# Optimization experiments

Measured on AMD Instinct MI355X. Metric: run time of the kernel, lower is better.

Reference implementation:

```python
import jax, jax.numpy as jnp
import numpy as np

B, C, H, W = 16, 128, 112, 112
OUTC = 256


def _conv(x, w, padding, groups=1, bias=None):
    y = jax.lax.conv_general_dilated(
        x, w, window_strides=(1, 1), padding=[(padding, padding), (padding, padding)],
        dimension_numbers=("NCHW", "OIHW", "NCHW"), feature_group_count=groups)
    if bias is not None:
        y = y + bias[None, :, None, None]
    return y


def _grid_sample_1ch(chan, g):
    # chan: [B,H,W] single channel; g: [B,H,W,2] with (x,y) in [-1,1].
    # PyTorch grid_sample: bilinear, zeros padding, align_corners=False.
    Bn, Hc, Wc = chan.shape
    ix = (g[..., 0] + 1.0) * (Wc * 0.5) - 0.5
    iy = (g[..., 1] + 1.0) * (Hc * 0.5) - 0.5
    x0 = jnp.floor(ix)
    y0 = jnp.floor(iy)
    wx = ix - x0
    wy = iy - y0
    x0i = x0.astype(jnp.int32)
    y0i = y0.astype(jnp.int32)
    flat = chan.reshape(Bn, -1)

    def gather(yi, xi):
        valid = (yi >= 0) & (yi < Hc) & (xi >= 0) & (xi < Wc)
        idx = jnp.clip(yi, 0, Hc - 1) * Wc + jnp.clip(xi, 0, Wc - 1)
        v = jnp.take_along_axis(flat, idx.reshape(Bn, -1), axis=1).reshape(idx.shape)
        return jnp.where(valid, v, 0.0)

    v00 = gather(y0i, x0i)
    v01 = gather(y0i, x0i + 1)
    v10 = gather(y0i + 1, x0i)
    v11 = gather(y0i + 1, x0i + 1)
    return (v00 * (1 - wx) * (1 - wy) + v01 * wx * (1 - wy)
            + v10 * (1 - wx) * wy + v11 * wx * wy)


def setup_inputs() -> dict:
    key = jax.random.key(0)
    k1, k2, k3, k4 = jax.random.split(key, 4)
    x = jax.random.normal(k1, (B, C, H, W), dtype=jnp.float32)
    depth_w = jax.random.normal(k2, (C, 1, 3, 3), dtype=jnp.float32) * 0.1
    point_w = jax.random.normal(k3, (OUTC, C, 1, 1), dtype=jnp.float32) * 0.05
    offset_w = jax.random.normal(k4, (2 * C, C, 3, 3), dtype=jnp.float32) * 0.02
    offset_b = jnp.zeros((2 * C,), dtype=jnp.float32)
    return {"x": x, "depth_w": depth_w, "point_w": point_w,
            "offset_w": offset_w, "offset_b": offset_b}


def reference(x, depth_w, point_w, offset_w, offset_b):
    offset = jnp.tanh(_conv(x, offset_w, padding=1, bias=offset_b))  # [B,2C,H,W]
    out = _conv(x, depth_w, padding=1, groups=C)                     # [B,C,H,W]

    # Base grid, matching np.meshgrid + np.repeat([C,C], axis=0):
    # channels 0..C-1 are all X, channels C..2C-1 are all Y.
    gX, gY = jnp.meshgrid(jnp.linspace(-1.0, 1.0, W), jnp.linspace(-1.0, 1.0, H), indexing="xy")
    grid = jnp.concatenate([gX[None], gY[None]], axis=0)  # [2,H,W]
    grid = jnp.repeat(grid, C, axis=0)                    # [2C,H,W]

    sg = jnp.clip(grid[None] + offset, -1.0, 1.0)         # [B,2C,H,W]
    sg = sg.transpose(0, 2, 3, 1)                         # [B,H,W,2C]
    sg = sg.reshape(B, H, W, C, 2).transpose(3, 0, 1, 2, 4)  # [C,B,H,W,2]

    chans = out.transpose(1, 0, 2, 3)                     # [C,B,H,W]
    sampled = jax.vmap(_grid_sample_1ch)(chans, sg)       # [C,B,H,W]
    sampled = sampled.transpose(1, 0, 2, 3)               # [B,C,H,W]

    return _conv(sampled, point_w, padding=0)             # [B,OUTC,H,W]
```

## Files before the change

### kernel.cpp

```cpp
#include <hip/hip_runtime.h>
#include <hip/hip_bf16.h>

#define B_    16
#define C_    128
#define H_    112
#define W_    112
#define OUTC_ 256
#define TWOC_ 256
#define HW_   (H_ * W_)
#define CHW_  ((size_t)C_ * HW_)

typedef __hip_bfloat16 bf16;
typedef short bf16x8 __attribute__((ext_vector_type(8)));
typedef short s16x4  __attribute__((ext_vector_type(4)));
typedef float f32x4  __attribute__((ext_vector_type(4)));

__device__ __forceinline__ float b2f(bf16 v) { return __bfloat162float(v); }
__device__ __forceinline__ bf16  f2b(float v) { return __float2bfloat16(v); }

__device__ __forceinline__ float rd(const float* p) { return *p; }
__device__ __forceinline__ float rd(const bf16* p)  { return b2f(*p); }
__device__ __forceinline__ void  wr(float* p, float v) { *p = v; }
__device__ __forceinline__ void  wr(bf16* p,  float v) { *p = f2b(v); }

__device__ __forceinline__ float fast_tanh(float v) {
    float e = __expf(2.f * v);
    return 1.f - 2.f / (e + 1.f);
}

__global__ __launch_bounds__(256) void k_probe(const unsigned short* __restrict__ x,
                                               int* __restrict__ flag) {
    __shared__ int cnt[256];
    int tid = threadIdx.x;
    int c = 0;
#pragma unroll
    for (int i = 0; i < 8; ++i) {
        unsigned short u = x[tid * 8 + i];
        int e = (u >> 7) & 0xFF;
        if (e >= 135) c++;
    }
    cnt[tid] = c;
    __syncthreads();
    if (tid == 0) {
        int s = 0;
        for (int i = 0; i < 256; ++i) s += cnt[i];
        *flag = (s > 64) ? 1 : 0;
    }
}

__global__ __launch_bounds__(256) void k_wprep(const void* __restrict__ ow,
                                               bf16* __restrict__ wth,
                                               bf16* __restrict__ wtl,
                                               const int* __restrict__ flag) {
    int i = blockIdx.x * 256 + threadIdx.x;
    if (i >= 9 * 4 * 256 * 32) return;
    int cp  = i & 31;
    int oc  = (i >> 5) & 255;
    int tcc = i >> 13;
    int cc  = tcc & 3;
    int tap = tcc >> 2;
    int c   = cc * 32 + cp;
    size_t src = ((size_t)oc * C_ + c) * 9 + tap;
    float v = (*flag) ? ((const float*)ow)[src] : b2f(((const bf16*)ow)[src]);
    bf16 hb = f2b(v);
    float lo = v - b2f(hb);
    wth[i] = hb;
    wtl[i] = f2b(lo);
}

__global__ __launch_bounds__(256) void k_pwprep(const void* __restrict__ pw,
                                                bf16* __restrict__ pwh,
                                                bf16* __restrict__ pwl,
                                                const int* __restrict__ flag) {
    int i = blockIdx.x * 256 + threadIdx.x;
    if (i >= 4 * 256 * 32) return;
    int cp   = i & 31;
    int oc   = (i >> 5) & 255;
    int cc   = i >> 13;
    int c    = cc * 32 + cp;
    size_t src = (size_t)oc * C_ + c;
    float v = (*flag) ? ((const float*)pw)[src] : b2f(((const bf16*)pw)[src]);
    bf16 hb = f2b(v);
    float lo = v - b2f(hb);
    pwh[i] = hb;
    pwl[i] = f2b(lo);
}

__global__ __launch_bounds__(256) void k_offset_mfma(
    const void* __restrict__ xsrc, const bf16* __restrict__ wth,
    const bf16* __restrict__ wtl, const void* __restrict__ ob,
    float* __restrict__ off, const int* __restrict__ flag)
{
    __shared__ alignas(16) short Sh[114 * 32];
    __shared__ alignas(16) short Sl[114 * 32];

    const int tid  = threadIdx.x;
    const int lane = tid & 63;
    const int wv   = tid >> 6;
    const int l15  = lane & 15;
    const int l4   = lane >> 4;
    const int hraw = blockIdx.x;
    const int h    = (hraw & 7) * 14 + (hraw >> 3);
    const int b    = blockIdx.y;
    const int fullp = *flag;

    const float* xf = (const float*)xsrc;
    const bf16*  xb = (const bf16*)xsrc;

    f32x4 acc[4][7];
    f32x4 zero = {0.f, 0.f, 0.f, 0.f};
#pragma unroll
    for (int m = 0; m < 4; ++m)
#pragma unroll
        for (int n = 0; n < 7; ++n) acc[m][n] = zero;

    for (int cc = 0; cc < 4; ++cc) {
        for (int kh = 0; kh < 3; ++kh) {
            const int row = h + kh - 1;
            const bool rowok = (row >= 0) && (row < H_);
            __syncthreads();
            for (int i = tid; i < 912; i += 256) {
                int n  = i % 114;
                int cq = i / 114;
                int col = n - 1;
                bool ok = rowok && (col >= 0) && (col < W_);
                size_t base = ((size_t)(b * C_ + cc * 32 + cq * 4)) * HW_
                            + (size_t)row * W_ + col;
                short hs[4], ls[4];
#pragma unroll
                for (int t = 0; t < 4; ++t) {
                    float v = 0.f;
                    if (ok) v = fullp ? xf[base + (size_t)t * HW_]
                                      : b2f(xb[base + (size_t)t * HW_]);
                    bf16 hb = f2b(v);
                    float hv = b2f(hb);
                    bf16 lb = f2b(v - hv);
                    hs[t] = *(short*)&hb;
                    ls[t] = *(short*)&lb;
                }
                int ob_ = (cq * 8) ^ (((n >> 1) & 3) << 4);
                int so  = n * 32 + (ob_ >> 1);
                s16x4 th, tl;
                th[0] = hs[0]; th[1] = hs[1]; th[2] = hs[2]; th[3] = hs[3];
                tl[0] = ls[0]; tl[1] = ls[1]; tl[2] = ls[2]; tl[3] = ls[3];
                *(s16x4*)&Sh[so] = th;
                *(s16x4*)&Sl[so] = tl;
            }
            __syncthreads();

            for (int kw = 0; kw < 3; ++kw) {
                const size_t wchunk = ((size_t)((kh * 3 + kw) * 4 + cc)) * (256 * 32);
                bf16x8 ah[4], al[4];
#pragma unroll
                for (int m = 0; m < 4; ++m) {
                    size_t aoff = (size_t)(wv * 64 + m * 16 + l15) * 32 + 8 * l4;
                    ah[m] = *(const bf16x8*)(wth + wchunk + aoff);
                }
                if (fullp) {
#pragma unroll
                    for (int m = 0; m < 4; ++m) {
                        size_t aoff = (size_t)(wv * 64 + m * 16 + l15) * 32 + 8 * l4;
                        al[m] = *(const bf16x8*)(wtl + wchunk + aoff);
                    }
                }
#pragma unroll
                for (int n = 0; n < 7; ++n) {
                    int rowb = n * 16 + l15 + kw;
                    int o2   = (16 * l4) ^ (((rowb >> 1) & 3) << 4);
                    int so   = rowb * 32 + (o2 >> 1);
                    bf16x8 xh = *(const bf16x8*)&Sh[so];
#pragma unroll
                    for (int m = 0; m < 4; ++m)
                        acc[m][n] = __builtin_amdgcn_mfma_f32_16x16x32_bf16(
                            ah[m], xh, acc[m][n], 0, 0, 0);
                    if (fullp) {
                        bf16x8 xl = *(const bf16x8*)&Sl[so];
#pragma unroll
                        for (int m = 0; m < 4; ++m)
                            acc[m][n] = __builtin_amdgcn_mfma_f32_16x16x32_bf16(
                                ah[m], xl, acc[m][n], 0, 0, 0);
#pragma unroll
                        for (int m = 0; m < 4; ++m)
                            acc[m][n] = __builtin_amdgcn_mfma_f32_16x16x32_bf16(
                                al[m], xh, acc[m][n], 0, 0, 0);
                    }
                }
            }
        }
    }

#pragma unroll
    for (int m = 0; m < 4; ++m) {
        int ocb = wv * 64 + m * 16 + l4 * 4;
        float bias[4];
#pragma unroll
        for (int j = 0; j < 4; ++j)
            bias[j] = fullp ? ((const float*)ob)[ocb + j]
                            : b2f(((const bf16*)ob)[ocb + j]);
#pragma unroll
        for (int n = 0; n < 7; ++n) {
            int w = n * 16 + l15;
#pragma unroll
            for (int j = 0; j < 4; ++j) {
                size_t o = ((size_t)(b * TWOC_ + ocb + j)) * HW_ + (size_t)h * W_ + w;
                off[o] = fast_tanh(acc[m][n][j] + bias[j]);
            }
        }
    }
}

template <typename TI>
__device__ void dw_body(const TI* __restrict__ x, const TI* __restrict__ dw,
                        bf16* __restrict__ out) {
    int hw = blockIdx.x * 256 + threadIdx.x;
    int c = blockIdx.y, b = blockIdx.z;
    int h = hw / W_, w = hw - h * W_;
    float wv[9];
#pragma unroll
    for (int k = 0; k < 9; ++k) wv[k] = rd(dw + c * 9 + k);
    const TI* xc = x + (size_t)b * CHW_ + (size_t)c * HW_;
    float acc = 0.f;
#pragma unroll
    for (int kh = 0; kh < 3; ++kh) {
        int hh = h + kh - 1;
        bool hv = (hh >= 0) && (hh < H_);
#pragma unroll
        for (int kw = 0; kw < 3; ++kw) {
            int ww = w + kw - 1;
            bool v = hv && (ww >= 0) && (ww < W_);
            acc += (v ? rd(xc + hh * W_ + ww) : 0.f) * wv[kh * 3 + kw];
        }
    }
    out[(size_t)(b * C_ + c) * HW_ + hw] = f2b(acc);
}

__global__ __launch_bounds__(256) void k_dw(const void* x, const void* dw,
                                            bf16* out, const int* flag) {
    if (*flag) dw_body<float>((const float*)x, (const float*)dw, out);
    else       dw_body<bf16>((const bf16*)x, (const bf16*)dw, out);
}

__global__ __launch_bounds__(256) void k_sample(
    const float* __restrict__ off, const bf16* __restrict__ dwout,
    bf16* __restrict__ samp) {
    int hw = blockIdx.x * 256 + threadIdx.x;
    int c = blockIdx.y, b = blockIdx.z;
    int h = hw / W_, w = hw - h * W_;

    float gbase = (c < 64) ? (-1.f + 2.f * (float)w / 111.f)
                           : (-1.f + 2.f * (float)h / 111.f);
    const float* offb = off + (size_t)b * TWOC_ * HW_;
    float ox = offb[(size_t)(2 * c) * HW_ + hw];
    float oy = offb[(size_t)(2 * c + 1) * HW_ + hw];
    float gx = fminf(fmaxf(gbase + ox, -1.f), 1.f);
    float gy = fminf(fmaxf(gbase + oy, -1.f), 1.f);
    float ix = (gx + 1.f) * 56.f - 0.5f;
    float iy = (gy + 1.f) * 56.f - 0.5f;
    float x0f = floorf(ix), y0f = floorf(iy);
    float wx = ix - x0f, wy = iy - y0f;
    int x0 = (int)x0f, y0 = (int)y0f;

    const bf16* p = dwout + (size_t)(b * C_ + c) * HW_;
    float v00 = 0.f, v01 = 0.f, v10 = 0.f, v11 = 0.f;
    bool y0v = (y0 >= 0) && (y0 < H_), y1v = (y0 + 1 >= 0) && (y0 + 1 < H_);
    bool x0v = (x0 >= 0) && (x0 < W_), x1v = (x0 + 1 >= 0) && (x0 + 1 < W_);
    if (y0v && x0v) v00 = b2f(p[y0 * W_ + x0]);
    if (y0v && x1v) v01 = b2f(p[y0 * W_ + x0 + 1]);
    if (y1v && x0v) v10 = b2f(p[(y0 + 1) * W_ + x0]);
    if (y1v && x1v) v11 = b2f(p[(y0 + 1) * W_ + x0 + 1]);

    float v = v00 * (1.f - wx) * (1.f - wy) + v01 * wx * (1.f - wy)
            + v10 * (1.f - wx) * wy + v11 * wx * wy;
    samp[(size_t)(b * C_ + c) * HW_ + hw] = f2b(v);
}

__global__ __launch_bounds__(256) void k_pw_mfma(
    const bf16* __restrict__ samp, const bf16* __restrict__ pwh,
    const bf16* __restrict__ pwl, void* __restrict__ out,
    const int* __restrict__ flag)
{
    const int tid  = threadIdx.x;
    const int lane = tid & 63;
    const int wv   = tid >> 6;
    const int l15  = lane & 15;
    const int l4   = lane >> 4;
    const int hraw = blockIdx.x;
    const int h    = (hraw & 7) * 14 + (hraw >> 3);
    const int b    = blockIdx.y;
    const int fullp = *flag;

    const bf16* srow = samp + (size_t)b * C_ * HW_ + (size_t)h * W_;

    f32x4 acc[4][7];
    f32x4 zero = {0.f, 0.f, 0.f, 0.f};
#pragma unroll
    for (int m = 0; m < 4; ++m)
#pragma unroll
        for (int n = 0; n < 7; ++n) acc[m][n] = zero;

    for (int cc = 0; cc < 4; ++cc) {
        bf16x8 ah[4], al[4];
#pragma unroll
        for (int m = 0; m < 4; ++m) {
            size_t aoff = ((size_t)cc * 256 + (wv * 64 + m * 16 + l15)) * 32 + 8 * l4;
            ah[m] = *(const bf16x8*)(pwh + aoff);
        }
        if (fullp) {
#pragma unroll
            for (int m = 0; m < 4; ++m) {
                size_t aoff = ((size_t)cc * 256 + (wv * 64 + m * 16 + l15)) * 32 + 8 * l4;
                al[m] = *(const bf16x8*)(pwl + aoff);
            }
        }
#pragma unroll
        for (int n = 0; n < 7; ++n) {
            int w = n * 16 + l15;
            const bf16* bp = srow + (size_t)(cc * 32 + 8 * l4) * HW_ + w;
            bf16x8 xv;
#pragma unroll
            for (int j = 0; j < 8; ++j) {
                bf16 t = bp[(size_t)j * HW_];
                xv[j] = *(short*)&t;
            }
#pragma unroll
            for (int m = 0; m < 4; ++m)
                acc[m][n] = __builtin_amdgcn_mfma_f32_16x16x32_bf16(
                    ah[m], xv, acc[m][n], 0, 0, 0);
            if (fullp) {
#pragma unroll
                for (int m = 0; m < 4; ++m)
                    acc[m][n] = __builtin_amdgcn_mfma_f32_16x16x32_bf16(
                        al[m], xv, acc[m][n], 0, 0, 0);
            }
        }
    }

#pragma unroll
    for (int m = 0; m < 4; ++m) {
        int ocb = wv * 64 + m * 16 + l4 * 4;
#pragma unroll
        for (int n = 0; n < 7; ++n) {
            int w = n * 16 + l15;
#pragma unroll
            for (int j = 0; j < 4; ++j) {
                size_t o = ((size_t)(b * OUTC_ + ocb + j)) * HW_ + (size_t)h * W_ + w;
                if (fullp) ((float*)out)[o] = acc[m][n][j];
                else       ((bf16*)out)[o]  = f2b(acc[m][n][j]);
            }
        }
    }
}

extern "C" void kernel_launch(void* const* d_in, const int* in_sizes, int n_in,
                              void* d_out, int out_size, void* d_ws, size_t ws_size,
                              hipStream_t stream) {
    (void)in_sizes; (void)n_in; (void)out_size; (void)ws_size;
    const void* x        = d_in[0];
    const void* depth_w  = d_in[1];
    const void* point_w  = d_in[2];
    const void* offset_w = d_in[3];
    const void* offset_b = d_in[4];

    char* ws = (char*)d_ws;
    int*   flag = (int*)ws;
    const size_t off_bytes = (size_t)B_ * TWOC_ * HW_ * 4;
    float* off  = (float*)(ws + 256);
    bf16*  wth  = (bf16*)(ws + 256 + off_bytes);
    bf16*  wtl  = wth + 9 * 4 * 256 * 32;
    bf16*  pwh  = wtl + 9 * 4 * 256 * 32;
    bf16*  pwl  = pwh + 4 * 256 * 32;
    bf16* dwout = pwl + 4 * 256 * 32;
    bf16* samp  = dwout + (size_t)B_ * C_ * HW_;

    k_probe      <<<1, 256, 0, stream>>>((const unsigned short*)x, flag);
    k_wprep      <<<1152, 256, 0, stream>>>(offset_w, wth, wtl, flag);
    k_pwprep     <<<128, 256, 0, stream>>>(point_w, pwh, pwl, flag);
    k_offset_mfma<<<dim3(H_, B_), 256, 0, stream>>>(x, wth, wtl, offset_b, off, flag);
    k_dw         <<<dim3(49, C_, B_), 256, 0, stream>>>(x, depth_w, dwout, flag);
    k_sample     <<<dim3(49, C_, B_), 256, 0, stream>>>(off, dwout, samp);
    k_pw_mfma    <<<dim3(H_, B_), 256, 0, stream>>>(samp, pwh, pwl, d_out, flag);
}
```

Baseline: 1.041 ms.

## Double-buffer offset conv input staging and stage pointwise input via LDS

```diff
diff --git a/kernel.cpp b/kernel.cpp
--- a/kernel.cpp
+++ b/kernel.cpp
@@ -20,8 +20,6 @@
 
 __device__ __forceinline__ float rd(const float* p) { return *p; }
 __device__ __forceinline__ float rd(const bf16* p)  { return b2f(*p); }
-__device__ __forceinline__ void  wr(float* p, float v) { *p = v; }
-__device__ __forceinline__ void  wr(bf16* p,  float v) { *p = f2b(v); }
 
 __device__ __forceinline__ float fast_tanh(float v) {
     float e = __expf(2.f * v);
@@ -91,8 +89,8 @@
     const bf16* __restrict__ wtl, const void* __restrict__ ob,
     float* __restrict__ off, const int* __restrict__ flag)
 {
-    __shared__ alignas(16) short Sh[114 * 32];
-    __shared__ alignas(16) short Sl[114 * 32];
+    __shared__ alignas(16) short Sh[2][114 * 32];
+    __shared__ alignas(16) short Sl[2][114 * 32];
 
     const int tid  = threadIdx.x;
     const int lane = tid & 63;
@@ -107,6 +105,17 @@
     const float* xf = (const float*)xsrc;
     const bf16*  xb = (const bf16*)xsrc;
 
+    int  nn[4], cq[4];
+    bool act[4];
+#pragma unroll
+    for (int t = 0; t < 4; ++t) {
+        int i = tid + 256 * t;
+        act[t] = (i < 912);
+        int ii = act[t] ? i : 0;
+        nn[t] = ii % 114;
+        cq[t] = ii / 114;
+    }
+
     f32x4 acc[4][7];
     f32x4 zero = {0.f, 0.f, 0.f, 0.f};
 #pragma unroll
@@ -114,79 +123,104 @@
 #pragma unroll
         for (int n = 0; n < 7; ++n) acc[m][n] = zero;
 
-    for (int cc = 0; cc < 4; ++cc) {
-        for (int kh = 0; kh < 3; ++kh) {
-            const int row = h + kh - 1;
-            const bool rowok = (row >= 0) && (row < H_);
-            __syncthreads();
-            for (int i = tid; i < 912; i += 256) {
-                int n  = i % 114;
-                int cq = i / 114;
-                int col = n - 1;
-                bool ok = rowok && (col >= 0) && (col < W_);
-                size_t base = ((size_t)(b * C_ + cc * 32 + cq * 4)) * HW_
-                            + (size_t)row * W_ + col;
-                short hs[4], ls[4];
-#pragma unroll
-                for (int t = 0; t < 4; ++t) {
-                    float v = 0.f;
-                    if (ok) v = fullp ? xf[base + (size_t)t * HW_]
-                                      : b2f(xb[base + (size_t)t * HW_]);
-                    bf16 hb = f2b(v);
-                    float hv = b2f(hb);
-                    bf16 lb = f2b(v - hv);
-                    hs[t] = *(short*)&hb;
-                    ls[t] = *(short*)&lb;
-                }
-                int ob_ = (cq * 8) ^ (((n >> 1) & 3) << 4);
-                int so  = n * 32 + (ob_ >> 1);
-                s16x4 th, tl;
-                th[0] = hs[0]; th[1] = hs[1]; th[2] = hs[2]; th[3] = hs[3];
-                tl[0] = ls[0]; tl[1] = ls[1]; tl[2] = ls[2]; tl[3] = ls[3];
-                *(s16x4*)&Sh[so] = th;
-                *(s16x4*)&Sl[so] = tl;
-            }
-            __syncthreads();
-
-            for (int kw = 0; kw < 3; ++kw) {
-                const size_t wchunk = ((size_t)((kh * 3 + kw) * 4 + cc)) * (256 * 32);
-                bf16x8 ah[4], al[4];
+    float vreg[4][4];
+
+    auto issue = [&](int s) {
+        int cc = s >> 2;
+        int kh = s - cc * 3;
+        cc = s / 3; kh = s - cc * 3;
+        int row = h + kh - 1;
+        bool rowok = (row >= 0) && (row < H_);
+#pragma unroll
+        for (int t = 0; t < 4; ++t) {
+            int col = nn[t] - 1;
+            bool ok = act[t] && rowok && (col >= 0) && (col < W_);
+            size_t base = ((size_t)(b * C_ + cc * 32 + cq[t] * 4)) * HW_
+                        + (size_t)row * W_ + col;
+#pragma unroll
+            for (int q = 0; q < 4; ++q) {
+                float v = 0.f;
+                if (ok) v = fullp ? xf[base + (size_t)q * HW_]
+                                  : b2f(xb[base + (size_t)q * HW_]);
+                vreg[t][q] = v;
+            }
+        }
+    };
+
+    auto writebuf = [&](int bi) {
+#pragma unroll
+        for (int t = 0; t < 4; ++t) {
+            if (!act[t]) continue;
+            short hs[4], ls[4];
+#pragma unroll
+            for (int q = 0; q < 4; ++q) {
+                float v = vreg[t][q];
+                bf16 hb = f2b(v);
+                float hv = b2f(hb);
+                bf16 lb = f2b(v - hv);
+                hs[q] = *(short*)&hb;
+                ls[q] = *(short*)&lb;
+            }
+            int n   = nn[t];
+            int ob_ = (cq[t] * 8) ^ (((n >> 1) & 3) << 4);
+            int so  = n * 32 + (ob_ >> 1);
+            s16x4 th, tl;
+            th[0] = hs[0]; th[1] = hs[1]; th[2] = hs[2]; th[3] = hs[3];
+            tl[0] = ls[0]; tl[1] = ls[1]; tl[2] = ls[2]; tl[3] = ls[3];
+            *(s16x4*)&Sh[bi][so] = th;
+            *(s16x4*)&Sl[bi][so] = tl;
+        }
+    };
+
+    issue(0);
+    writebuf(0);
+
+    for (int s = 0; s < 12; ++s) {
+        const int cc = s / 3;
+        const int kh = s - cc * 3;
+        if (s < 11) issue(s + 1);
+        __syncthreads();
+        const short* Bh = Sh[s & 1];
+        const short* Bl = Sl[s & 1];
+        for (int kw = 0; kw < 3; ++kw) {
+            const size_t wchunk = ((size_t)((kh * 3 + kw) * 4 + cc)) * (256 * 32);
+            bf16x8 ah[4], al[4];
+#pragma unroll
+            for (int m = 0; m < 4; ++m) {
+                size_t aoff = (size_t)(wv * 64 + m * 16 + l15) * 32 + 8 * l4;
+                ah[m] = *(const bf16x8*)(wth + wchunk + aoff);
+            }
+            if (fullp) {
 #pragma unroll
                 for (int m = 0; m < 4; ++m) {
                     size_t aoff = (size_t)(wv * 64 + m * 16 + l15) * 32 + 8 * l4;
-                    ah[m] = *(const bf16x8*)(wth + wchunk + aoff);
+                    al[m] = *(const bf16x8*)(wtl + wchunk + aoff);
                 }
+            }
+#pragma unroll
+            for (int n = 0; n < 7; ++n) {
+                int rowb = n * 16 + l15 + kw;
+                int o2   = (16 * l4) ^ (((rowb >> 1) & 3) << 4);
+                int so   = rowb * 32 + (o2 >> 1);
+                bf16x8 xh = *(const bf16x8*)&Bh[so];
+#pragma unroll
+                for (int m = 0; m < 4; ++m)
+                    acc[m][n] = __builtin_amdgcn_mfma_f32_16x16x32_bf16(
+                        ah[m], xh, acc[m][n], 0, 0, 0);
                 if (fullp) {
-#pragma unroll
-                    for (int m = 0; m < 4; ++m) {
-                        size_t aoff = (size_t)(wv * 64 + m * 16 + l15) * 32 + 8 * l4;
-                        al[m] = *(const bf16x8*)(wtl + wchunk + aoff);
-                    }
-                }
-#pragma unroll
-                for (int n = 0; n < 7; ++n) {
-                    int rowb = n * 16 + l15 + kw;
-                    int o2   = (16 * l4) ^ (((rowb >> 1) & 3) << 4);
-                    int so   = rowb * 32 + (o2 >> 1);
-                    bf16x8 xh = *(const bf16x8*)&Sh[so];
+                    bf16x8 xl = *(const bf16x8*)&Bl[so];
 #pragma unroll
                     for (int m = 0; m < 4; ++m)
                         acc[m][n] = __builtin_amdgcn_mfma_f32_16x16x32_bf16(
-                            ah[m], xh, acc[m][n], 0, 0, 0);
-                    if (fullp) {
-                        bf16x8 xl = *(const bf16x8*)&Sl[so];
-#pragma unroll
-                        for (int m = 0; m < 4; ++m)
-                            acc[m][n] = __builtin_amdgcn_mfma_f32_16x16x32_bf16(
-                                ah[m], xl, acc[m][n], 0, 0, 0);
-#pragma unroll
-                        for (int m = 0; m < 4; ++m)
-                            acc[m][n] = __builtin_amdgcn_mfma_f32_16x16x32_bf16(
-                                al[m], xh, acc[m][n], 0, 0, 0);
-                    }
+                            ah[m], xl, acc[m][n], 0, 0, 0);
+#pragma unroll
+                    for (int m = 0; m < 4; ++m)
+                        acc[m][n] = __builtin_amdgcn_mfma_f32_16x16x32_bf16(
+                            al[m], xh, acc[m][n], 0, 0, 0);
                 }
             }
         }
+        if (s < 11) writebuf((s + 1) & 1);
     }
 
 #pragma unroll
@@ -279,6 +313,8 @@
     const bf16* __restrict__ pwl, void* __restrict__ out,
     const int* __restrict__ flag)
 {
+    __shared__ short SP[C_ * 114];
+
     const int tid  = threadIdx.x;
     const int lane = tid & 63;
     const int wv   = tid >> 6;
@@ -291,6 +327,18 @@
 
     const bf16* srow = samp + (size_t)b * C_ * HW_ + (size_t)h * W_;
 
+#pragma unroll
+    for (int it = 0; it < 7; ++it) {
+        int i  = it * 256 + tid;
+        int c  = i / 14;
+        int wc = i - c * 14;
+        bf16x8 v = *(const bf16x8*)(srow + (size_t)c * HW_ + wc * 8);
+        short* d = &SP[c * 114 + wc * 8];
+#pragma unroll
+        for (int t = 0; t < 8; ++t) d[t] = v[t];
+    }
+    __syncthreads();
+
     f32x4 acc[4][7];
     f32x4 zero = {0.f, 0.f, 0.f, 0.f};
 #pragma unroll
@@ -312,16 +360,13 @@
                 al[m] = *(const bf16x8*)(pwl + aoff);
             }
         }
+        const int c0 = cc * 32 + 8 * l4;
 #pragma unroll
         for (int n = 0; n < 7; ++n) {
             int w = n * 16 + l15;
-            const bf16* bp = srow + (size_t)(cc * 32 + 8 * l4) * HW_ + w;
             bf16x8 xv;
 #pragma unroll
-            for (int j = 0; j < 8; ++j) {
-                bf16 t = bp[(size_t)j * HW_];
-                xv[j] = *(short*)&t;
-            }
+            for (int j = 0; j < 8; ++j) xv[j] = SP[(c0 + j) * 114 + w];
 #pragma unroll
             for (int m = 0; m < 4; ++m)
                 acc[m][n] = __builtin_amdgcn_mfma_f32_16x16x32_bf16(
```

Result: slower. 1.127 ms (+8.2%).
